# Kernel optimization log

Measured on AMD Instinct MI355X. Metric: run time of the kernel, lower is better.

Reference implementation:

```python
import jax, jax.numpy as jnp
import numpy as np

B, S, D, UNITS = 4, 512, 256, 128
NEG = -1e9


def setup_inputs() -> dict:
    key = jax.random.key(0)
    k1, k2, k3, k4 = jax.random.split(key, 4)
    values = jax.random.normal(k1, (B, S, D), dtype=jnp.float32)
    Wq = jax.random.normal(k2, (D, UNITS), dtype=jnp.float32) * (1.0 / np.sqrt(D))
    Wv = jax.random.normal(k3, (D, UNITS), dtype=jnp.float32) * (1.0 / np.sqrt(D))
    Vw = jax.random.normal(k4, (UNITS,), dtype=jnp.float32) * (1.0 / np.sqrt(UNITS))
    return {"values": values, "Wq": Wq, "Wv": Wv, "Vw": Vw}


def reference(values, Wq, Wv, Vw):
    # values: [B, S, D]
    query = values @ Wq            # [B, S, U]
    value = values @ Wv            # [B, S, U]
    # additive (Bahdanau) score: V . tanh(q_i + v_j) -> [B, S, S]
    feat = jnp.tanh(query[:, :, None, :] + value[:, None, :, :])  # [B,S,S,U]
    score = jnp.einsum('biju,u->bij', feat, Vw)
    seq_len = values.shape[1]
    causal = jnp.tril(jnp.ones((seq_len, seq_len), dtype=jnp.float32))  # lower-tri = visible
    score = score + (1.0 - causal)[None, :, :] * jnp.asarray(NEG, score.dtype)
    attn = jax.nn.softmax(score, axis=-1)          # [B, S, S]
    context = jnp.matmul(attn, values)             # [B, S, D]
    return context
```

## Files before the change

### kernel.cpp

```cpp
#include <hip/hip_runtime.h>
#include <hip/hip_fp16.h>

#define SEQ 512
#define DIM 256
#define UN  128
#define BSZ 2048
#define CSC 2.8853900817779268f

struct h8 { __half2 a, b, c, d; };

static __device__ __forceinline__ unsigned short f2bf(float x) {
  unsigned u = __float_as_uint(x);
  u += 0x7FFF + ((u >> 16) & 1);
  return (unsigned short)(u >> 16);
}
static __device__ __forceinline__ float bf2f(unsigned short s) {
  return __uint_as_float((unsigned)s << 16);
}

__global__ __launch_bounds__(256) void proj_kernel(
    const float* __restrict__ values, const float* __restrict__ Wq,
    const float* __restrict__ Wv, float* __restrict__ Eq,
    unsigned short* __restrict__ Ev, __half* __restrict__ Vf16) {
  __shared__ float vsm[4 * DIM];
  const int t = threadIdx.x;
  const int r0 = blockIdx.x * 4;
  {
    const int row = t >> 6, c4 = (t & 63) * 4;
    const float4 v = *(const float4*)(values + (r0 + row) * DIM + c4);
    *(float4*)&vsm[row * DIM + c4] = v;
    __half2* vf = (__half2*)(Vf16 + (r0 + row) * DIM + c4);
    vf[0] = __floats2half2_rn(v.x, v.y);
    vf[1] = __floats2half2_rn(v.z, v.w);
  }
  __syncthreads();
  const int half = t >> 7, u = t & 127;
  const float* __restrict__ W = half ? Wv : Wq;
  float acc[4] = {0.f, 0.f, 0.f, 0.f};
  for (int d = 0; d < DIM; d += 4) {
    const float w0 = W[(d + 0) * UN + u], w1 = W[(d + 1) * UN + u];
    const float w2 = W[(d + 2) * UN + u], w3 = W[(d + 3) * UN + u];
#pragma unroll
    for (int k = 0; k < 4; ++k) {
      const float4 v = *(const float4*)&vsm[k * DIM + d];
      acc[k] = fmaf(v.x, w0, acc[k]);
      acc[k] = fmaf(v.y, w1, acc[k]);
      acc[k] = fmaf(v.z, w2, acc[k]);
      acc[k] = fmaf(v.w, w3, acc[k]);
    }
  }
  if (!half) {
#pragma unroll
    for (int k = 0; k < 4; ++k)
      Eq[(r0 + k) * UN + u] = __builtin_amdgcn_exp2f(acc[k] * CSC);
  } else {
    ushort4 o;
    o.x = f2bf(__builtin_amdgcn_exp2f(acc[0] * CSC));
    o.y = f2bf(__builtin_amdgcn_exp2f(acc[1] * CSC));
    o.z = f2bf(__builtin_amdgcn_exp2f(acc[2] * CSC));
    o.w = f2bf(__builtin_amdgcn_exp2f(acc[3] * CSC));
    *(ushort4*)(Ev + (size_t)u * BSZ + r0) = o;
  }
}

__global__ __launch_bounds__(256, 4) void attn_kernel(
    const __half* __restrict__ Vf16, const float* __restrict__ Eq,
    const unsigned short* __restrict__ Ev, const float* __restrict__ Vw,
    float* __restrict__ out) {
  __shared__ float sc[2 * SEQ];
  __shared__ float scp[2 * SEQ];
  __shared__ float part[8 * DIM];
  __shared__ float invs[2];

  const int t = threadIdx.x;
  const int b = blockIdx.x >> 8, p = blockIdx.x & 255;
  const int bS = b * SEQ;
  const int i = p;
  const int ihi = SEQ - 1 - p;
  const int jhi = ihi;

  const float* __restrict__ eql = Eq + (bS + i) * UN;
  const float* __restrict__ eqh = Eq + (bS + ihi) * UN;

  {
    const int qd = t & 127, jb = qd << 2;
    const int u0 = (t >> 7) << 6;
    float* __restrict__ so = (t >> 7) ? scp : sc;
    const unsigned short* __restrict__ evp = Ev + (size_t)u0 * BSZ + bS + jb;
    if ((t & 64) == 0) {
      float h0=0.f,h1=0.f,h2=0.f,h3=0.f,l0=0.f,l1=0.f,l2=0.f,l3=0.f;
      ushort4 ec = *(const ushort4*)evp;
#pragma unroll 4
      for (int k = 0; k < 64; ++k) {
        const ushort4 en = *(const ushort4*)(evp + (size_t)(k + 1) * BSZ);
        const float qh = eqh[u0 + k], ql = eql[u0 + k], w = Vw[u0 + k];
        const float e0 = bf2f(ec.x), e1 = bf2f(ec.y), e2 = bf2f(ec.z), e3 = bf2f(ec.w);
        h0 = fmaf(w, __builtin_amdgcn_rcpf(fmaf(qh, e0, 1.f)), h0);
        h1 = fmaf(w, __builtin_amdgcn_rcpf(fmaf(qh, e1, 1.f)), h1);
        h2 = fmaf(w, __builtin_amdgcn_rcpf(fmaf(qh, e2, 1.f)), h2);
        h3 = fmaf(w, __builtin_amdgcn_rcpf(fmaf(qh, e3, 1.f)), h3);
        l0 = fmaf(w, __builtin_amdgcn_rcpf(fmaf(ql, e0, 1.f)), l0);
        l1 = fmaf(w, __builtin_amdgcn_rcpf(fmaf(ql, e1, 1.f)), l1);
        l2 = fmaf(w, __builtin_amdgcn_rcpf(fmaf(ql, e2, 1.f)), l2);
        l3 = fmaf(w, __builtin_amdgcn_rcpf(fmaf(ql, e3, 1.f)), l3);
        ec = en;
      }
      *(float4*)&so[SEQ + jb] = make_float4(h0, h1, h2, h3);
      *(float4*)&so[jb]       = make_float4(l0, l1, l2, l3);
    } else if (jb <= jhi) {
      float h0=0.f,h1=0.f,h2=0.f,h3=0.f;
      ushort4 ec = *(const ushort4*)evp;
#pragma unroll 4
      for (int k = 0; k < 64; ++k) {
        const ushort4 en = *(const ushort4*)(evp + (size_t)(k + 1) * BSZ);
        const float qh = eqh[u0 + k], w = Vw[u0 + k];
        h0 = fmaf(w, __builtin_amdgcn_rcpf(fmaf(qh, bf2f(ec.x), 1.f)), h0);
        h1 = fmaf(w, __builtin_amdgcn_rcpf(fmaf(qh, bf2f(ec.y), 1.f)), h1);
        h2 = fmaf(w, __builtin_amdgcn_rcpf(fmaf(qh, bf2f(ec.z), 1.f)), h2);
        h3 = fmaf(w, __builtin_amdgcn_rcpf(fmaf(qh, bf2f(ec.w), 1.f)), h3);
        ec = en;
      }
      *(float4*)&so[SEQ + jb] = make_float4(h0, h1, h2, h3);
    }
  }
  __syncthreads();

  {
    const int w = t >> 6, l = t & 63;
    if (w < 2) {
      const int jmax = (w == 0) ? i : jhi;
      float* __restrict__ r0p = sc + w * SEQ;
      const float* __restrict__ r1p = scp + w * SEQ;
      float m = 1e30f;
      for (int j = l; j <= jmax; j += 64) m = fminf(m, r0p[j] + r1p[j]);
#pragma unroll
      for (int o = 32; o; o >>= 1) m = fminf(m, __shfl_xor(m, o));
      float sum = 0.f;
      for (int j = l; j <= jmax; j += 64) {
        const float pr = __builtin_amdgcn_exp2f((m - (r0p[j] + r1p[j])) * CSC);
        r0p[j] = pr;
        sum += pr;
      }
#pragma unroll
      for (int o = 32; o; o >>= 1) sum += __shfl_xor(sum, o);
      if (l == 0) invs[w] = __builtin_amdgcn_rcpf(sum);
    }
  }
  __syncthreads();

  {
    const int g = t >> 6, l = t & 63;
    const int jo = l >> 5, d8 = (l & 31) << 3;
    float alo[8], ahi[8];
#pragma unroll
    for (int k = 0; k < 8; ++k) { alo[k] = 0.f; ahi[k] = 0.f; }
    int j = 2 * g + jo;
    h8 vc = *(const h8*)(Vf16 + (size_t)(bS + j) * DIM + d8);
    for (; j <= i; j += 8) {
      const int jn = (j + 8 <= jhi) ? j + 8 : jhi;
      const h8 vn = *(const h8*)(Vf16 + (size_t)(bS + jn) * DIM + d8);
      const float plo = sc[j], phi = sc[SEQ + j];
      const float2 f0 = __half22float2(vc.a), f1 = __half22float2(vc.b);
      const float2 f2 = __half22float2(vc.c), f3 = __half22float2(vc.d);
      alo[0] = fmaf(plo, f0.x, alo[0]); alo[1] = fmaf(plo, f0.y, alo[1]);
      alo[2] = fmaf(plo, f1.x, alo[2]); alo[3] = fmaf(plo, f1.y, alo[3]);
      alo[4] = fmaf(plo, f2.x, alo[4]); alo[5] = fmaf(plo, f2.y, alo[5]);
      alo[6] = fmaf(plo, f3.x, alo[6]); alo[7] = fmaf(plo, f3.y, alo[7]);
      ahi[0] = fmaf(phi, f0.x, ahi[0]); ahi[1] = fmaf(phi, f0.y, ahi[1]);
      ahi[2] = fmaf(phi, f1.x, ahi[2]); ahi[3] = fmaf(phi, f1.y, ahi[3]);
      ahi[4] = fmaf(phi, f2.x, ahi[4]); ahi[5] = fmaf(phi, f2.y, ahi[5]);
      ahi[6] = fmaf(phi, f3.x, ahi[6]); ahi[7] = fmaf(phi, f3.y, ahi[7]);
      vc = vn;
    }
    for (; j <= jhi; j += 8) {
      const int jn = (j + 8 <= jhi) ? j + 8 : jhi;
      const h8 vn = *(const h8*)(Vf16 + (size_t)(bS + jn) * DIM + d8);
      const float phi = sc[SEQ + j];
      const float2 f0 = __half22float2(vc.a), f1 = __half22float2(vc.b);
      const float2 f2 = __half22float2(vc.c), f3 = __half22float2(vc.d);
      ahi[0] = fmaf(phi, f0.x, ahi[0]); ahi[1] = fmaf(phi, f0.y, ahi[1]);
      ahi[2] = fmaf(phi, f1.x, ahi[2]); ahi[3] = fmaf(phi, f1.y, ahi[3]);
      ahi[4] = fmaf(phi, f2.x, ahi[4]); ahi[5] = fmaf(phi, f2.y, ahi[5]);
      ahi[6] = fmaf(phi, f3.x, ahi[6]); ahi[7] = fmaf(phi, f3.y, ahi[7]);
      vc = vn;
    }
#pragma unroll
    for (int k = 0; k < 8; ++k) {
      alo[k] += __shfl_xor(alo[k], 32);
      ahi[k] += __shfl_xor(ahi[k], 32);
    }
    if (jo == 0) {
      float* __restrict__ plo_ = &part[(g * 2 + 0) * DIM + d8];
      float* __restrict__ phi_ = &part[(g * 2 + 1) * DIM + d8];
      *(float4*)(plo_ + 0) = make_float4(alo[0], alo[1], alo[2], alo[3]);
      *(float4*)(plo_ + 4) = make_float4(alo[4], alo[5], alo[6], alo[7]);
      *(float4*)(phi_ + 0) = make_float4(ahi[0], ahi[1], ahi[2], ahi[3]);
      *(float4*)(phi_ + 4) = make_float4(ahi[4], ahi[5], ahi[6], ahi[7]);
    }
  }
  __syncthreads();

  {
    const float olo = (part[0 * DIM + t] + part[2 * DIM + t] +
                       part[4 * DIM + t] + part[6 * DIM + t]) * invs[0];
    const float ohi = (part[1 * DIM + t] + part[3 * DIM + t] +
                       part[5 * DIM + t] + part[7 * DIM + t]) * invs[1];
    out[(bS + i) * DIM + t] = olo;
    out[(bS + ihi) * DIM + t] = ohi;
  }
}

extern "C" void kernel_launch(void* const* d_in, const int* in_sizes, int n_in,
                              void* d_out, int out_size, void* d_ws, size_t ws_size,
                              hipStream_t stream) {
  const float* values = (const float*)d_in[0];
  const float* Wq     = (const float*)d_in[1];
  const float* Wv     = (const float*)d_in[2];
  const float* Vw     = (const float*)d_in[3];
  float* out = (float*)d_out;
  float* Eq = (float*)d_ws;
  unsigned short* Ev = (unsigned short*)(Eq + (size_t)BSZ * UN);
  __half* Vf16 = (__half*)(Ev + (size_t)UN * BSZ);
  proj_kernel<<<dim3(BSZ / 4), 256, 0, stream>>>(values, Wq, Wv, Eq, Ev, Vf16);
  attn_kernel<<<dim3(4 * 256), 256, 0, stream>>>(Vf16, Eq, Ev, Vw, out);
}
```

Baseline: 105.4 us.

## Split paired-row attention blocks into one query row per block

Each attention block now handles a single query row instead of a pair of rows (i and S-1-i) that shared Ev and V loads. The grid doubles to 2048 blocks, interleaving short and long rows, and launch bounds raise occupancy to 8 blocks per CU. Softmax now uses all four waves with a shared-memory reduction instead of two waves. The change gives up the Ev/V reuse across the row pair, so global and L2 traffic rises, in exchange for finer-grained load balance and lower per-block register and LDS use.

```diff
diff --git a/kernel.cpp b/kernel.cpp
--- a/kernel.cpp
+++ b/kernel.cpp
@@ -63,151 +63,106 @@
   }
 }
 
-__global__ __launch_bounds__(256, 4) void attn_kernel(
+__global__ __launch_bounds__(256, 8) void attn_kernel(
     const __half* __restrict__ Vf16, const float* __restrict__ Eq,
     const unsigned short* __restrict__ Ev, const float* __restrict__ Vw,
     float* __restrict__ out) {
-  __shared__ float sc[2 * SEQ];
-  __shared__ float scp[2 * SEQ];
-  __shared__ float part[8 * DIM];
-  __shared__ float invs[2];
+  __shared__ float sc[SEQ];
+  __shared__ float scp[SEQ];
+  __shared__ float part[4 * DIM];
+  __shared__ float red[8];
 
   const int t = threadIdx.x;
-  const int b = blockIdx.x >> 8, p = blockIdx.x & 255;
+  const int b = blockIdx.x >> 9;
+  const int idx = blockIdx.x & 511;
+  const int i = (idx & 1) ? (SEQ - 1 - (idx >> 1)) : (idx >> 1);
   const int bS = b * SEQ;
-  const int i = p;
-  const int ihi = SEQ - 1 - p;
-  const int jhi = ihi;
 
-  const float* __restrict__ eql = Eq + (bS + i) * UN;
-  const float* __restrict__ eqh = Eq + (bS + ihi) * UN;
+  const float* __restrict__ eqr = Eq + (size_t)(bS + i) * UN;
 
   {
-    const int qd = t & 127, jb = qd << 2;
+    const int jb = (t & 127) << 2;
     const int u0 = (t >> 7) << 6;
-    float* __restrict__ so = (t >> 7) ? scp : sc;
-    const unsigned short* __restrict__ evp = Ev + (size_t)u0 * BSZ + bS + jb;
-    if ((t & 64) == 0) {
-      float h0=0.f,h1=0.f,h2=0.f,h3=0.f,l0=0.f,l1=0.f,l2=0.f,l3=0.f;
+    if (jb <= i) {
+      float* __restrict__ so = (t >> 7) ? scp : sc;
+      const unsigned short* __restrict__ evp = Ev + (size_t)u0 * BSZ + bS + jb;
+      float s0 = 0.f, s1 = 0.f, s2 = 0.f, s3 = 0.f;
       ushort4 ec = *(const ushort4*)evp;
 #pragma unroll 4
       for (int k = 0; k < 64; ++k) {
         const ushort4 en = *(const ushort4*)(evp + (size_t)(k + 1) * BSZ);
-        const float qh = eqh[u0 + k], ql = eql[u0 + k], w = Vw[u0 + k];
-        const float e0 = bf2f(ec.x), e1 = bf2f(ec.y), e2 = bf2f(ec.z), e3 = bf2f(ec.w);
-        h0 = fmaf(w, __builtin_amdgcn_rcpf(fmaf(qh, e0, 1.f)), h0);
-        h1 = fmaf(w, __builtin_amdgcn_rcpf(fmaf(qh, e1, 1.f)), h1);
-        h2 = fmaf(w, __builtin_amdgcn_rcpf(fmaf(qh, e2, 1.f)), h2);
-        h3 = fmaf(w, __builtin_amdgcn_rcpf(fmaf(qh, e3, 1.f)), h3);
-        l0 = fmaf(w, __builtin_amdgcn_rcpf(fmaf(ql, e0, 1.f)), l0);
-        l1 = fmaf(w, __builtin_amdgcn_rcpf(fmaf(ql, e1, 1.f)), l1);
-        l2 = fmaf(w, __builtin_amdgcn_rcpf(fmaf(ql, e2, 1.f)), l2);
-        l3 = fmaf(w, __builtin_amdgcn_rcpf(fmaf(ql, e3, 1.f)), l3);
+        const float q = eqr[u0 + k], w = Vw[u0 + k];
+        s0 = fmaf(w, __builtin_amdgcn_rcpf(fmaf(q, bf2f(ec.x), 1.f)), s0);
+        s1 = fmaf(w, __builtin_amdgcn_rcpf(fmaf(q, bf2f(ec.y), 1.f)), s1);
+        s2 = fmaf(w, __builtin_amdgcn_rcpf(fmaf(q, bf2f(ec.z), 1.f)), s2);
+        s3 = fmaf(w, __builtin_amdgcn_rcpf(fmaf(q, bf2f(ec.w), 1.f)), s3);
         ec = en;
       }
-      *(float4*)&so[SEQ + jb] = make_float4(h0, h1, h2, h3);
-      *(float4*)&so[jb]       = make_float4(l0, l1, l2, l3);
-    } else if (jb <= jhi) {
-      float h0=0.f,h1=0.f,h2=0.f,h3=0.f;
-      ushort4 ec = *(const ushort4*)evp;
-#pragma unroll 4
-      for (int k = 0; k < 64; ++k) {
-        const ushort4 en = *(const ushort4*)(evp + (size_t)(k + 1) * BSZ);
-        const float qh = eqh[u0 + k], w = Vw[u0 + k];
-        h0 = fmaf(w, __builtin_amdgcn_rcpf(fmaf(qh, bf2f(ec.x), 1.f)), h0);
-        h1 = fmaf(w, __builtin_amdgcn_rcpf(fmaf(qh, bf2f(ec.y), 1.f)), h1);
-        h2 = fmaf(w, __builtin_amdgcn_rcpf(fmaf(qh, bf2f(ec.z), 1.f)), h2);
-        h3 = fmaf(w, __builtin_amdgcn_rcpf(fmaf(qh, bf2f(ec.w), 1.f)), h3);
-        ec = en;
-      }
-      *(float4*)&so[SEQ + jb] = make_float4(h0, h1, h2, h3);
+      *(float4*)&so[jb] = make_float4(s0, s1, s2, s3);
     }
   }
   __syncthreads();
 
   {
     const int w = t >> 6, l = t & 63;
-    if (w < 2) {
-      const int jmax = (w == 0) ? i : jhi;
-      float* __restrict__ r0p = sc + w * SEQ;
-      const float* __restrict__ r1p = scp + w * SEQ;
-      float m = 1e30f;
-      for (int j = l; j <= jmax; j += 64) m = fminf(m, r0p[j] + r1p[j]);
+    const float sA = (t <= i) ? sc[t] + scp[t] : 1e30f;
+    const float sB = (t + 256 <= i) ? sc[t + 256] + scp[t + 256] : 1e30f;
+    float m = fminf(sA, sB);
 #pragma unroll
-      for (int o = 32; o; o >>= 1) m = fminf(m, __shfl_xor(m, o));
-      float sum = 0.f;
-      for (int j = l; j <= jmax; j += 64) {
-        const float pr = __builtin_amdgcn_exp2f((m - (r0p[j] + r1p[j])) * CSC);
-        r0p[j] = pr;
-        sum += pr;
+    for (int o = 32; o; o >>= 1) m = fminf(m, __shfl_xor(m, o));
+    if (l == 0) red[w] = m;
+    __syncthreads();
+    m = fminf(fminf(red[0], red[1]), fminf(red[2], red[3]));
+    float sum = 0.f;
+    if (t <= i) {
+      const float p = __builtin_amdgcn_exp2f((m - sA) * CSC);
+      sc[t] = p; sum += p;
+    }
+    if (t + 256 <= i) {
+      const float p = __builtin_amdgcn_exp2f((m - sB) * CSC);
+      sc[t + 256] = p; sum += p;
+    }
+#pragma unroll
+    for (int o = 32; o; o >>= 1) sum += __shfl_xor(sum, o);
+    if (l == 0) red[4 + w] = sum;
+  }
+  __syncthreads();
+  const float inv = __builtin_amdgcn_rcpf(red[4] + red[5] + red[6] + red[7]);
+
+  {
+    const int g = t >> 6, l = t & 63;
+    const int jo = l >> 5, d8 = (l & 31) << 3;
+    float a[8];
+#pragma unroll
+    for (int k = 0; k < 8; ++k) a[k] = 0.f;
+    int j = 2 * g + jo;
+    if (j <= i) {
+      h8 vc = *(const h8*)(Vf16 + (size_t)(bS + j) * DIM + d8);
+      for (; j <= i; j += 8) {
+        const int jn = (j + 8 <= i) ? j + 8 : i;
+        const h8 vn = *(const h8*)(Vf16 + (size_t)(bS + jn) * DIM + d8);
+        const float p = sc[j];
+        const float2 f0 = __half22float2(vc.a), f1 = __half22float2(vc.b);
+        const float2 f2 = __half22float2(vc.c), f3 = __half22float2(vc.d);
+        a[0] = fmaf(p, f0.x, a[0]); a[1] = fmaf(p, f0.y, a[1]);
+        a[2] = fmaf(p, f1.x, a[2]); a[3] = fmaf(p, f1.y, a[3]);
+        a[4] = fmaf(p, f2.x, a[4]); a[5] = fmaf(p, f2.y, a[5]);
+        a[6] = fmaf(p, f3.x, a[6]); a[7] = fmaf(p, f3.y, a[7]);
+        vc = vn;
       }
+    }
 #pragma unroll
-      for (int o = 32; o; o >>= 1) sum += __shfl_xor(sum, o);
-      if (l == 0) invs[w] = __builtin_amdgcn_rcpf(sum);
+    for (int k = 0; k < 8; ++k) a[k] += __shfl_xor(a[k], 32);
+    if (jo == 0) {
+      float* __restrict__ pp = &part[g * DIM + d8];
+      *(float4*)(pp + 0) = make_float4(a[0], a[1], a[2], a[3]);
+      *(float4*)(pp + 4) = make_float4(a[4], a[5], a[6], a[7]);
     }
   }
   __syncthreads();
 
-  {
-    const int g = t >> 6, l = t & 63;
-    const int jo = l >> 5, d8 = (l & 31) << 3;
-    float alo[8], ahi[8];
-#pragma unroll
-    for (int k = 0; k < 8; ++k) { alo[k] = 0.f; ahi[k] = 0.f; }
-    int j = 2 * g + jo;
-    h8 vc = *(const h8*)(Vf16 + (size_t)(bS + j) * DIM + d8);
-    for (; j <= i; j += 8) {
-      const int jn = (j + 8 <= jhi) ? j + 8 : jhi;
-      const h8 vn = *(const h8*)(Vf16 + (size_t)(bS + jn) * DIM + d8);
-      const float plo = sc[j], phi = sc[SEQ + j];
-      const float2 f0 = __half22float2(vc.a), f1 = __half22float2(vc.b);
-      const float2 f2 = __half22float2(vc.c), f3 = __half22float2(vc.d);
-      alo[0] = fmaf(plo, f0.x, alo[0]); alo[1] = fmaf(plo, f0.y, alo[1]);
-      alo[2] = fmaf(plo, f1.x, alo[2]); alo[3] = fmaf(plo, f1.y, alo[3]);
-      alo[4] = fmaf(plo, f2.x, alo[4]); alo[5] = fmaf(plo, f2.y, alo[5]);
-      alo[6] = fmaf(plo, f3.x, alo[6]); alo[7] = fmaf(plo, f3.y, alo[7]);
-      ahi[0] = fmaf(phi, f0.x, ahi[0]); ahi[1] = fmaf(phi, f0.y, ahi[1]);
-      ahi[2] = fmaf(phi, f1.x, ahi[2]); ahi[3] = fmaf(phi, f1.y, ahi[3]);
-      ahi[4] = fmaf(phi, f2.x, ahi[4]); ahi[5] = fmaf(phi, f2.y, ahi[5]);
-      ahi[6] = fmaf(phi, f3.x, ahi[6]); ahi[7] = fmaf(phi, f3.y, ahi[7]);
-      vc = vn;
-    }
-    for (; j <= jhi; j += 8) {
-      const int jn = (j + 8 <= jhi) ? j + 8 : jhi;
-      const h8 vn = *(const h8*)(Vf16 + (size_t)(bS + jn) * DIM + d8);
-      const float phi = sc[SEQ + j];
-      const float2 f0 = __half22float2(vc.a), f1 = __half22float2(vc.b);
-      const float2 f2 = __half22float2(vc.c), f3 = __half22float2(vc.d);
-      ahi[0] = fmaf(phi, f0.x, ahi[0]); ahi[1] = fmaf(phi, f0.y, ahi[1]);
-      ahi[2] = fmaf(phi, f1.x, ahi[2]); ahi[3] = fmaf(phi, f1.y, ahi[3]);
-      ahi[4] = fmaf(phi, f2.x, ahi[4]); ahi[5] = fmaf(phi, f2.y, ahi[5]);
-      ahi[6] = fmaf(phi, f3.x, ahi[6]); ahi[7] = fmaf(phi, f3.y, ahi[7]);
-      vc = vn;
-    }
-#pragma unroll
-    for (int k = 0; k < 8; ++k) {
-      alo[k] += __shfl_xor(alo[k], 32);
-      ahi[k] += __shfl_xor(ahi[k], 32);
-    }
-    if (jo == 0) {
-      float* __restrict__ plo_ = &part[(g * 2 + 0) * DIM + d8];
-      float* __restrict__ phi_ = &part[(g * 2 + 1) * DIM + d8];
-      *(float4*)(plo_ + 0) = make_float4(alo[0], alo[1], alo[2], alo[3]);
-      *(float4*)(plo_ + 4) = make_float4(alo[4], alo[5], alo[6], alo[7]);
-      *(float4*)(phi_ + 0) = make_float4(ahi[0], ahi[1], ahi[2], ahi[3]);
-      *(float4*)(phi_ + 4) = make_float4(ahi[4], ahi[5], ahi[6], ahi[7]);
-    }
-  }
-  __syncthreads();
-
-  {
-    const float olo = (part[0 * DIM + t] + part[2 * DIM + t] +
-                       part[4 * DIM + t] + part[6 * DIM + t]) * invs[0];
-    const float ohi = (part[1 * DIM + t] + part[3 * DIM + t] +
-                       part[5 * DIM + t] + part[7 * DIM + t]) * invs[1];
-    out[(bS + i) * DIM + t] = olo;
-    out[(bS + ihi) * DIM + t] = ohi;
-  }
+  out[(size_t)(bS + i) * DIM + t] =
+      (part[t] + part[DIM + t] + part[2 * DIM + t] + part[3 * DIM + t]) * inv;
 }
 
 extern "C" void kernel_launch(void* const* d_in, const int* in_sizes, int n_in,
@@ -222,5 +177,5 @@
   unsigned short* Ev = (unsigned short*)(Eq + (size_t)BSZ * UN);
   __half* Vf16 = (__half*)(Ev + (size_t)UN * BSZ);
   proj_kernel<<<dim3(BSZ / 4), 256, 0, stream>>>(values, Wq, Wv, Eq, Ev, Vf16);
-  attn_kernel<<<dim3(4 * 256), 256, 0, stream>>>(Vf16, Eq, Ev, Vw, out);
+  attn_kernel<<<dim3(BSZ), 256, 0, stream>>>(Vf16, Eq, Ev, Vw, out);
 }
```

Measured after the change: 115.2 us. +9.3%, slower.
